# Optimization experiments

Measured on AMD Instinct MI355X. Metric: run time of the kernel, lower is better.

## Reference

```python
import jax, jax.numpy as jnp
import numpy as np


def setup_inputs() -> dict:
    key = jax.random.key(0)
    ks = jax.random.split(key, 6)
    b, t, s, qu, vu, d = 8, 64, 512, 512, 512, 512
    return {
        "query": jax.random.normal(ks[0], (b, t, qu), jnp.float32),
        "value": jax.random.normal(ks[1], (b, s, vu), jnp.float32),
        "mask": jax.random.randint(ks[2], (b, s), 0, 2).astype(bool),
        "W1_w": jax.random.normal(ks[3], (qu, d), jnp.float32) * (1.0 / np.sqrt(qu)),
        "W1_b": jnp.zeros((d,), jnp.float32),
        "W2_w": jax.random.normal(ks[4], (vu, d), jnp.float32) * (1.0 / np.sqrt(vu)),
        "W2_b": jnp.zeros((d,), jnp.float32),
        "scale": jax.random.normal(ks[5], (d,), jnp.float32) * 0.05,
    }


def reference(query, value, mask, W1_w, W1_b, W2_w, W2_b, scale):
    # Dense projections
    q = jnp.einsum('btq,qd->btd', query, W1_w) + W1_b   # [b,t,d]
    k = jnp.einsum('bsv,vd->bsd', value, W2_w) + W2_b   # [b,s,d]
    # Additive (Bahdanau) score with learned scale vector (Keras use_scale=True)
    # scores[b,t,s] = sum_d scale[d] * tanh(q[b,t,d] + k[b,s,d])
    scores = jnp.einsum('btsd,d->bts', jnp.tanh(q[:, :, None, :] + k[:, None, :, :]), scale)
    # Mask over source positions (value mask); query mask is all-ones (no-op)
    scores = jnp.where(mask[:, None, :], scores, jnp.float32(-1e9))
    attention_weights = jax.nn.softmax(scores, axis=-1)   # [b,t,s]
    context_vector = jnp.einsum('bts,bsv->btv', attention_weights, value)  # [b,t,vu]
    return context_vector, attention_weights
```

## Files before the change

kernel.cpp:

```cpp
#include <hip/hip_runtime.h>
#include <hip/hip_bf16.h>

#define B_  8
#define T_  64
#define S_  512
#define D_  512

#define QN (512 * 512)
#define KN (4096 * 512)

#define TLOG2E 2.8853900817779268f
#define LOG2E  1.4426950408889634f

typedef __attribute__((ext_vector_type(8))) short bf16x8;
typedef __attribute__((ext_vector_type(4))) float f32x4;

__device__ __forceinline__ unsigned int pk2(float a, float b) {
    float2 f; f.x = a; f.y = b;
    __hip_bfloat162 h = __float22bfloat162_rn(f);
    return *(unsigned int*)&h;
}

__global__ __launch_bounds__(256) void mfma_gemm(
    const float* __restrict__ query, const float* __restrict__ value,
    const float* __restrict__ W1, const float* __restrict__ W2,
    const float* __restrict__ b1, const float* __restrict__ b2,
    float* __restrict__ qproj, float* __restrict__ kproj)
{
    __shared__ __align__(16) unsigned short Ab[64][40];
    __shared__ __align__(16) unsigned short Bs[64][40];

    const int x = blockIdx.x;
    const float *A, *W;
    float* C;
    int tm, tn;
    bool isq;
    if (x < 512) {
        tm = (x & 7) * 8 + ((x >> 3) & 7);
        tn = x >> 6;
        A = value; W = W2; C = kproj; isq = false;
    } else {
        int r = x - 512;
        tm = r >> 3; tn = r & 7;
        A = query; W = W1; C = qproj; isq = true;
    }

    const int tid  = threadIdx.x;
    const int lane = tid & 63;
    const int wid  = tid >> 6;
    const int wm = (wid & 1) * 32, wn = (wid >> 1) * 32;
    const int fm = lane & 15, fq = lane >> 4;

    f32x4 acc00 = {0.f, 0.f, 0.f, 0.f};
    f32x4 acc01 = acc00, acc10 = acc00, acc11 = acc00;

    const int ar = tid >> 2;
    const int ac = (tid & 3) * 8;
    const float* Ag = A + (size_t)(tm * 64 + ar) * 512 + ac;
    const int c0 = (tid & 15) * 4;
    const int kp = (tid >> 4) * 2;
    const float* Wg = W + (size_t)kp * 512 + tn * 64 + c0;

    float4 av0 = *(const float4*)(Ag);
    float4 av1 = *(const float4*)(Ag + 4);
    float4 wv0 = *(const float4*)(Wg);
    float4 wv1 = *(const float4*)(Wg + 512);

    for (int k0 = 0; k0 < 512; k0 += 32) {
        __syncthreads();
        {
            uint4 pa;
            pa.x = pk2(av0.x, av0.y); pa.y = pk2(av0.z, av0.w);
            pa.z = pk2(av1.x, av1.y); pa.w = pk2(av1.z, av1.w);
            *(uint4*)&Ab[ar][ac] = pa;
            *(unsigned int*)&Bs[c0 + 0][kp] = pk2(wv0.x, wv1.x);
            *(unsigned int*)&Bs[c0 + 1][kp] = pk2(wv0.y, wv1.y);
            *(unsigned int*)&Bs[c0 + 2][kp] = pk2(wv0.z, wv1.z);
            *(unsigned int*)&Bs[c0 + 3][kp] = pk2(wv0.w, wv1.w);
        }
        __syncthreads();
        const int kn = (k0 + 32) & 511;
        av0 = *(const float4*)(Ag + kn);
        av1 = *(const float4*)(Ag + kn + 4);
        wv0 = *(const float4*)(Wg + (size_t)kn * 512);
        wv1 = *(const float4*)(Wg + (size_t)kn * 512 + 512);

        bf16x8 a0  = *(const bf16x8*)&Ab[wm + fm][fq * 8];
        bf16x8 a1  = *(const bf16x8*)&Ab[wm + 16 + fm][fq * 8];
        bf16x8 b0  = *(const bf16x8*)&Bs[wn + fm][fq * 8];
        bf16x8 b1v = *(const bf16x8*)&Bs[wn + 16 + fm][fq * 8];
        acc00 = __builtin_amdgcn_mfma_f32_16x16x32_bf16(a0, b0,  acc00, 0, 0, 0);
        acc01 = __builtin_amdgcn_mfma_f32_16x16x32_bf16(a0, b1v, acc01, 0, 0, 0);
        acc10 = __builtin_amdgcn_mfma_f32_16x16x32_bf16(a1, b0,  acc10, 0, 0, 0);
        acc11 = __builtin_amdgcn_mfma_f32_16x16x32_bf16(a1, b1v, acc11, 0, 0, 0);
    }

    const int n0 = tn * 64 + wn + fm;
    const int n1 = n0 + 16;
    float bias0 = 0.f, bias1 = 0.f;
    if (isq) {
        bias0 = b1[n0] + b2[n0];
        bias1 = b1[n1] + b2[n1];
    }
    const int m0 = tm * 64 + wm + fq * 4;
#pragma unroll
    for (int r = 0; r < 4; ++r) {
        C[(size_t)(m0 + r) * 512 + n0]      = (acc00[r] + bias0) * TLOG2E;
        C[(size_t)(m0 + r) * 512 + n1]      = (acc01[r] + bias1) * TLOG2E;
        C[(size_t)(m0 + 16 + r) * 512 + n0] = (acc10[r] + bias0) * TLOG2E;
        C[(size_t)(m0 + 16 + r) * 512 + n1] = (acc11[r] + bias1) * TLOG2E;
    }
}

__global__ __launch_bounds__(512, 2) void fused_attn(
    const float* __restrict__ qproj, const float* __restrict__ kproj,
    const int*   __restrict__ mask,  const float* __restrict__ scale,
    const float* __restrict__ value,
    float* __restrict__ ctx, float* __restrict__ attn)
{
    const int blk = blockIdx.x;
    const int b  = blk & 7;
    const int tp = blk >> 3;
    const size_t row0 = (size_t)(b * T_ + tp * 2);

    __shared__ __align__(16) float q0A[512];
    __shared__ __align__(16) float dA[512];
    __shared__ __align__(16) float cA[512];
    __shared__ __align__(16) float2 wp2[512];
    __shared__ __align__(16) float4 part[2][4][128];
    __shared__ float2 red2[16];

    const int tid  = threadIdx.x;
    const int lane = tid & 63;
    const int wid  = tid >> 6;

    {
        float q0v = qproj[row0 * D_ + tid];
        float q1v = qproj[(row0 + 1) * D_ + tid];
        q0A[tid] = q0v;
        dA[tid]  = __builtin_amdgcn_exp2f(q1v - q0v);
        cA[tid]  = scale[tid];
    }
    __syncthreads();

    const int s = tid;
    const int m = mask[b * S_ + s];
    const float* kr = kproj + (size_t)(b * S_ + s) * D_;
    float p0 = 0.f, p1 = 0.f;

    float4 kf0 = ((const float4*)kr)[0];
    float4 kf1 = ((const float4*)kr)[1];
    float4 kf2 = ((const float4*)kr)[2];
    float4 kf3 = ((const float4*)kr)[3];

#define SC_STEP(K4, DD) do {                                                  \
        float4 q4 = *(const float4*)&q0A[DD];                                 \
        float4 dl = *(const float4*)&dA[DD];                                  \
        float4 c4 = *(const float4*)&cA[DD];                                  \
        float e, ra, rb;                                                      \
        e  = __builtin_amdgcn_exp2f(q4.x + (K4).x);                           \
        ra = __builtin_amdgcn_rcpf(e + 1.0f);                                 \
        rb = __builtin_amdgcn_rcpf(fmaf(e, dl.x, 1.0f));                      \
        p0 = fmaf(c4.x, ra, p0); p1 = fmaf(c4.x, rb, p1);                     \
        e  = __builtin_amdgcn_exp2f(q4.y + (K4).y);                           \
        ra = __builtin_amdgcn_rcpf(e + 1.0f);                                 \
        rb = __builtin_amdgcn_rcpf(fmaf(e, dl.y, 1.0f));                      \
        p0 = fmaf(c4.y, ra, p0); p1 = fmaf(c4.y, rb, p1);                     \
        e  = __builtin_amdgcn_exp2f(q4.z + (K4).z);                           \
        ra = __builtin_amdgcn_rcpf(e + 1.0f);                                 \
        rb = __builtin_amdgcn_rcpf(fmaf(e, dl.z, 1.0f));                      \
        p0 = fmaf(c4.z, ra, p0); p1 = fmaf(c4.z, rb, p1);                     \
        e  = __builtin_amdgcn_exp2f(q4.w + (K4).w);                           \
        ra = __builtin_amdgcn_rcpf(e + 1.0f);                                 \
        rb = __builtin_amdgcn_rcpf(fmaf(e, dl.w, 1.0f));                      \
        p0 = fmaf(c4.w, ra, p0); p1 = fmaf(c4.w, rb, p1);                     \
    } while (0)

    for (int c = 0; c < 32; ++c) {
        const int nx = ((c + 1) & 31) * 16;
        float4 nf0 = ((const float4*)(kr + nx))[0];
        float4 nf1 = ((const float4*)(kr + nx))[1];
        float4 nf2 = ((const float4*)(kr + nx))[2];
        float4 nf3 = ((const float4*)(kr + nx))[3];
        const int d0 = c * 16;
        SC_STEP(kf0, d0);
        SC_STEP(kf1, d0 + 4);
        SC_STEP(kf2, d0 + 8);
        SC_STEP(kf3, d0 + 12);
        kf0 = nf0; kf1 = nf1; kf2 = nf2; kf3 = nf3;
    }
#undef SC_STEP

    float x0 = m ? (-2.0f * p0) : -1e9f;
    float x1 = m ? (-2.0f * p1) : -1e9f;

    float2 mx; mx.x = x0; mx.y = x1;
#pragma unroll
    for (int off = 32; off >= 1; off >>= 1) {
        mx.x = fmaxf(mx.x, __shfl_xor(mx.x, off));
        mx.y = fmaxf(mx.y, __shfl_xor(mx.y, off));
    }
    if (lane == 0) red2[wid] = mx;
    __syncthreads();
    float2 M = red2[0];
#pragma unroll
    for (int i = 1; i < 8; ++i) {
        M.x = fmaxf(M.x, red2[i].x);
        M.y = fmaxf(M.y, red2[i].y);
    }

    float e0 = __builtin_amdgcn_exp2f((x0 - M.x) * LOG2E);
    float e1 = __builtin_amdgcn_exp2f((x1 - M.y) * LOG2E);
    float2 sm; sm.x = e0; sm.y = e1;
#pragma unroll
    for (int off = 32; off >= 1; off >>= 1) {
        sm.x += __shfl_xor(sm.x, off);
        sm.y += __shfl_xor(sm.y, off);
    }
    if (lane == 0) red2[8 + wid] = sm;
    __syncthreads();
    float2 SS = red2[8];
#pragma unroll
    for (int i = 9; i < 16; ++i) {
        SS.x += red2[i].x;
        SS.y += red2[i].y;
    }
    const float inv0 = __builtin_amdgcn_rcpf(SS.x);
    const float inv1 = __builtin_amdgcn_rcpf(SS.y);
    const float w0 = e0 * inv0, w1 = e1 * inv1;

    float2 wpair; wpair.x = w0; wpair.y = w1;
    wp2[s] = wpair;
    attn[row0 * S_ + s]       = w0;
    attn[(row0 + 1) * S_ + s] = w1;
    __syncthreads();

    const int g  = tid >> 7;
    const int v4 = tid & 127;
    const float* vb = value + ((size_t)(b * S_) + g * 128) * D_ + v4 * 4;
    float4 a0; a0.x = 0.f; a0.y = 0.f; a0.z = 0.f; a0.w = 0.f;
    float4 a1 = a0;
#pragma unroll 4
    for (int i = 0; i < 128; ++i) {
        float4 vv = *(const float4*)(vb + (size_t)i * D_);
        float2 w = wp2[g * 128 + i];
        a0.x = fmaf(w.x, vv.x, a0.x); a0.y = fmaf(w.x, vv.y, a0.y);
        a0.z = fmaf(w.x, vv.z, a0.z); a0.w = fmaf(w.x, vv.w, a0.w);
        a1.x = fmaf(w.y, vv.x, a1.x); a1.y = fmaf(w.y, vv.y, a1.y);
        a1.z = fmaf(w.y, vv.z, a1.z); a1.w = fmaf(w.y, vv.w, a1.w);
    }
    part[0][g][v4] = a0;
    part[1][g][v4] = a1;
    __syncthreads();
    if (tid < 256) {
        const int t = tid >> 7, v = tid & 127;
        float4 p0v = part[t][0][v], p1v = part[t][1][v];
        float4 p2v = part[t][2][v], p3v = part[t][3][v];
        float4 o;
        o.x = (p0v.x + p1v.x) + (p2v.x + p3v.x);
        o.y = (p0v.y + p1v.y) + (p2v.y + p3v.y);
        o.z = (p0v.z + p1v.z) + (p2v.z + p3v.z);
        o.w = (p0v.w + p1v.w) + (p2v.w + p3v.w);
        *(float4*)(ctx + (row0 + t) * D_ + v * 4) = o;
    }
}

extern "C" void kernel_launch(void* const* d_in, const int* in_sizes, int n_in,
                              void* d_out, int out_size, void* d_ws, size_t ws_size,
                              hipStream_t stream) {
    const float* query = (const float*)d_in[0];
    const float* value = (const float*)d_in[1];
    const int*   mask  = (const int*)  d_in[2];
    const float* W1w   = (const float*)d_in[3];
    const float* W1b   = (const float*)d_in[4];
    const float* W2w   = (const float*)d_in[5];
    const float* W2b   = (const float*)d_in[6];
    const float* scale = (const float*)d_in[7];

    float* ctx  = (float*)d_out;
    float* attn = (float*)d_out + (size_t)B_ * T_ * D_;

    float* qproj = (float*)d_ws;
    float* kproj = qproj + (size_t)QN;

    mfma_gemm<<<576, 256, 0, stream>>>(query, value, W1w, W2w, W1b, W2b,
                                       qproj, kproj);
    fused_attn<<<256, 512, 0, stream>>>(qproj, kproj, mask, scale, value,
                                        ctx, attn);
}
```

Baseline: 136.3 us.

## Split attention score D-reduction across 1024 threads and double-buffer GEMM LDS

```diff
diff --git a/kernel.cpp b/kernel.cpp
--- a/kernel.cpp
+++ b/kernel.cpp
@@ -27,8 +27,8 @@
     const float* __restrict__ b1, const float* __restrict__ b2,
     float* __restrict__ qproj, float* __restrict__ kproj)
 {
-    __shared__ __align__(16) unsigned short Ab[64][40];
-    __shared__ __align__(16) unsigned short Bs[64][40];
+    __shared__ __align__(16) unsigned short Ab[2][64][40];
+    __shared__ __align__(16) unsigned short Bs[2][64][40];
 
     const int x = blockIdx.x;
     const float *A, *W;
@@ -61,39 +61,52 @@
     const int kp = (tid >> 4) * 2;
     const float* Wg = W + (size_t)kp * 512 + tn * 64 + c0;
 
-    float4 av0 = *(const float4*)(Ag);
-    float4 av1 = *(const float4*)(Ag + 4);
-    float4 wv0 = *(const float4*)(Wg);
-    float4 wv1 = *(const float4*)(Wg + 512);
-
-    for (int k0 = 0; k0 < 512; k0 += 32) {
-        __syncthreads();
-        {
-            uint4 pa;
-            pa.x = pk2(av0.x, av0.y); pa.y = pk2(av0.z, av0.w);
-            pa.z = pk2(av1.x, av1.y); pa.w = pk2(av1.z, av1.w);
-            *(uint4*)&Ab[ar][ac] = pa;
-            *(unsigned int*)&Bs[c0 + 0][kp] = pk2(wv0.x, wv1.x);
-            *(unsigned int*)&Bs[c0 + 1][kp] = pk2(wv0.y, wv1.y);
-            *(unsigned int*)&Bs[c0 + 2][kp] = pk2(wv0.z, wv1.z);
-            *(unsigned int*)&Bs[c0 + 3][kp] = pk2(wv0.w, wv1.w);
-        }
-        __syncthreads();
-        const int kn = (k0 + 32) & 511;
-        av0 = *(const float4*)(Ag + kn);
-        av1 = *(const float4*)(Ag + kn + 4);
-        wv0 = *(const float4*)(Wg + (size_t)kn * 512);
-        wv1 = *(const float4*)(Wg + (size_t)kn * 512 + 512);
-
-        bf16x8 a0  = *(const bf16x8*)&Ab[wm + fm][fq * 8];
-        bf16x8 a1  = *(const bf16x8*)&Ab[wm + 16 + fm][fq * 8];
-        bf16x8 b0  = *(const bf16x8*)&Bs[wn + fm][fq * 8];
-        bf16x8 b1v = *(const bf16x8*)&Bs[wn + 16 + fm][fq * 8];
+    float4 av0, av1, wv0, wv1;
+
+#define STAGE(BUF) do {                                                       \
+        uint4 pa;                                                             \
+        pa.x = pk2(av0.x, av0.y); pa.y = pk2(av0.z, av0.w);                   \
+        pa.z = pk2(av1.x, av1.y); pa.w = pk2(av1.z, av1.w);                   \
+        *(uint4*)&Ab[BUF][ar][ac] = pa;                                       \
+        *(unsigned int*)&Bs[BUF][c0 + 0][kp] = pk2(wv0.x, wv1.x);             \
+        *(unsigned int*)&Bs[BUF][c0 + 1][kp] = pk2(wv0.y, wv1.y);             \
+        *(unsigned int*)&Bs[BUF][c0 + 2][kp] = pk2(wv0.z, wv1.z);             \
+        *(unsigned int*)&Bs[BUF][c0 + 3][kp] = pk2(wv0.w, wv1.w);             \
+    } while (0)
+
+    av0 = *(const float4*)(Ag);
+    av1 = *(const float4*)(Ag + 4);
+    wv0 = *(const float4*)(Wg);
+    wv1 = *(const float4*)(Wg + 512);
+    STAGE(0);
+    av0 = *(const float4*)(Ag + 32);
+    av1 = *(const float4*)(Ag + 36);
+    wv0 = *(const float4*)(Wg + 32 * 512);
+    wv1 = *(const float4*)(Wg + 33 * 512);
+    __syncthreads();
+
+#pragma unroll
+    for (int i = 0; i < 16; ++i) {
+        const int cur = i & 1, nxt = cur ^ 1;
+        bf16x8 a0  = *(const bf16x8*)&Ab[cur][wm + fm][fq * 8];
+        bf16x8 a1  = *(const bf16x8*)&Ab[cur][wm + 16 + fm][fq * 8];
+        bf16x8 b0  = *(const bf16x8*)&Bs[cur][wn + fm][fq * 8];
+        bf16x8 b1v = *(const bf16x8*)&Bs[cur][wn + 16 + fm][fq * 8];
+        if (i < 15) {
+            STAGE(nxt);
+            const int kn = ((i + 2) & 15) * 32;
+            av0 = *(const float4*)(Ag + kn);
+            av1 = *(const float4*)(Ag + kn + 4);
+            wv0 = *(const float4*)(Wg + (size_t)kn * 512);
+            wv1 = *(const float4*)(Wg + (size_t)kn * 512 + 512);
+        }
         acc00 = __builtin_amdgcn_mfma_f32_16x16x32_bf16(a0, b0,  acc00, 0, 0, 0);
         acc01 = __builtin_amdgcn_mfma_f32_16x16x32_bf16(a0, b1v, acc01, 0, 0, 0);
         acc10 = __builtin_amdgcn_mfma_f32_16x16x32_bf16(a1, b0,  acc10, 0, 0, 0);
         acc11 = __builtin_amdgcn_mfma_f32_16x16x32_bf16(a1, b1v, acc11, 0, 0, 0);
-    }
+        __syncthreads();
+    }
+#undef STAGE
 
     const int n0 = tn * 64 + wn + fm;
     const int n1 = n0 + 16;
@@ -112,7 +125,7 @@
     }
 }
 
-__global__ __launch_bounds__(512, 2) void fused_attn(
+__global__ __launch_bounds__(1024) void fused_attn(
     const float* __restrict__ qproj, const float* __restrict__ kproj,
     const int*   __restrict__ mask,  const float* __restrict__ scale,
     const float* __restrict__ value,
@@ -126,15 +139,16 @@
     __shared__ __align__(16) float q0A[512];
     __shared__ __align__(16) float dA[512];
     __shared__ __align__(16) float cA[512];
+    __shared__ __align__(16) float2 pex[512];
     __shared__ __align__(16) float2 wp2[512];
-    __shared__ __align__(16) float4 part[2][4][128];
+    __shared__ __align__(16) float4 part[2][8][128];
     __shared__ float2 red2[16];
 
     const int tid  = threadIdx.x;
     const int lane = tid & 63;
     const int wid  = tid >> 6;
 
-    {
+    if (tid < 512) {
         float q0v = qproj[row0 * D_ + tid];
         float q1v = qproj[(row0 + 1) * D_ + tid];
         q0A[tid] = q0v;
@@ -143,9 +157,11 @@
     }
     __syncthreads();
 
-    const int s = tid;
+    const int s    = tid & 511;
+    const int half = tid >> 9;
+    const int dlo  = half << 8;
     const int m = mask[b * S_ + s];
-    const float* kr = kproj + (size_t)(b * S_ + s) * D_;
+    const float* kr = kproj + (size_t)(b * S_ + s) * D_ + dlo;
     float p0 = 0.f, p1 = 0.f;
 
     float4 kf0 = ((const float4*)kr)[0];
@@ -176,13 +192,13 @@
         p0 = fmaf(c4.w, ra, p0); p1 = fmaf(c4.w, rb, p1);                     \
     } while (0)
 
-    for (int c = 0; c < 32; ++c) {
-        const int nx = ((c + 1) & 31) * 16;
+    for (int c = 0; c < 16; ++c) {
+        const int nx = ((c + 1) & 15) * 16;
         float4 nf0 = ((const float4*)(kr + nx))[0];
         float4 nf1 = ((const float4*)(kr + nx))[1];
         float4 nf2 = ((const float4*)(kr + nx))[2];
         float4 nf3 = ((const float4*)(kr + nx))[3];
-        const int d0 = c * 16;
+        const int d0 = dlo + c * 16;
         SC_STEP(kf0, d0);
         SC_STEP(kf1, d0 + 4);
         SC_STEP(kf2, d0 + 8);
@@ -191,59 +207,70 @@
     }
 #undef SC_STEP
 
-    float x0 = m ? (-2.0f * p0) : -1e9f;
-    float x1 = m ? (-2.0f * p1) : -1e9f;
-
-    float2 mx; mx.x = x0; mx.y = x1;
-#pragma unroll
-    for (int off = 32; off >= 1; off >>= 1) {
-        mx.x = fmaxf(mx.x, __shfl_xor(mx.x, off));
-        mx.y = fmaxf(mx.y, __shfl_xor(mx.y, off));
-    }
-    if (lane == 0) red2[wid] = mx;
-    __syncthreads();
-    float2 M = red2[0];
-#pragma unroll
-    for (int i = 1; i < 8; ++i) {
-        M.x = fmaxf(M.x, red2[i].x);
-        M.y = fmaxf(M.y, red2[i].y);
-    }
-
-    float e0 = __builtin_amdgcn_exp2f((x0 - M.x) * LOG2E);
-    float e1 = __builtin_amdgcn_exp2f((x1 - M.y) * LOG2E);
-    float2 sm; sm.x = e0; sm.y = e1;
-#pragma unroll
-    for (int off = 32; off >= 1; off >>= 1) {
-        sm.x += __shfl_xor(sm.x, off);
-        sm.y += __shfl_xor(sm.y, off);
-    }
-    if (lane == 0) red2[8 + wid] = sm;
-    __syncthreads();
-    float2 SS = red2[8];
-#pragma unroll
-    for (int i = 9; i < 16; ++i) {
-        SS.x += red2[i].x;
-        SS.y += red2[i].y;
-    }
-    const float inv0 = __builtin_amdgcn_rcpf(SS.x);
-    const float inv1 = __builtin_amdgcn_rcpf(SS.y);
-    const float w0 = e0 * inv0, w1 = e1 * inv1;
-
-    float2 wpair; wpair.x = w0; wpair.y = w1;
-    wp2[s] = wpair;
-    attn[row0 * S_ + s]       = w0;
-    attn[(row0 + 1) * S_ + s] = w1;
+    if (half == 1) { float2 pp; pp.x = p0; pp.y = p1; pex[s] = pp; }
+    __syncthreads();
+
+    float x0 = 0.f, x1 = 0.f;
+    if (tid < 512) {
+        float2 ph = pex[s];
+        p0 += ph.x; p1 += ph.y;
+        x0 = m ? (-2.0f * p0) : -1e9f;
+        x1 = m ? (-2.0f * p1) : -1e9f;
+        float2 mx; mx.x = x0; mx.y = x1;
+#pragma unroll
+        for (int off = 32; off >= 1; off >>= 1) {
+            mx.x = fmaxf(mx.x, __shfl_xor(mx.x, off));
+            mx.y = fmaxf(mx.y, __shfl_xor(mx.y, off));
+        }
+        if (lane == 0) red2[wid] = mx;
+    }
+    __syncthreads();
+
+    float e0 = 0.f, e1 = 0.f;
+    if (tid < 512) {
+        float2 M = red2[0];
+#pragma unroll
+        for (int i = 1; i < 8; ++i) {
+            M.x = fmaxf(M.x, red2[i].x);
+            M.y = fmaxf(M.y, red2[i].y);
+        }
+        e0 = __builtin_amdgcn_exp2f((x0 - M.x) * LOG2E);
+        e1 = __builtin_amdgcn_exp2f((x1 - M.y) * LOG2E);
+        float2 sm; sm.x = e0; sm.y = e1;
+#pragma unroll
+        for (int off = 32; off >= 1; off >>= 1) {
+            sm.x += __shfl_xor(sm.x, off);
+            sm.y += __shfl_xor(sm.y, off);
+        }
+        if (lane == 0) red2[8 + wid] = sm;
+    }
+    __syncthreads();
+
+    if (tid < 512) {
+        float2 SS = red2[8];
+#pragma unroll
+        for (int i = 9; i < 16; ++i) {
+            SS.x += red2[i].x;
+            SS.y += red2[i].y;
+        }
+        const float w0 = e0 * __builtin_amdgcn_rcpf(SS.x);
+        const float w1 = e1 * __builtin_amdgcn_rcpf(SS.y);
+        float2 wpair; wpair.x = w0; wpair.y = w1;
+        wp2[s] = wpair;
+        attn[row0 * S_ + s]       = w0;
+        attn[(row0 + 1) * S_ + s] = w1;
+    }
     __syncthreads();
 
     const int g  = tid >> 7;
     const int v4 = tid & 127;
-    const float* vb = value + ((size_t)(b * S_) + g * 128) * D_ + v4 * 4;
+    const float* vb = value + ((size_t)(b * S_) + g * 64) * D_ + v4 * 4;
     float4 a0; a0.x = 0.f; a0.y = 0.f; a0.z = 0.f; a0.w = 0.f;
     float4 a1 = a0;
 #pragma unroll 4
-    for (int i = 0; i < 128; ++i) {
+    for (int i = 0; i < 64; ++i) {
         float4 vv = *(const float4*)(vb + (size_t)i * D_);
-        float2 w = wp2[g * 128 + i];
+        float2 w = wp2[g * 64 + i];
         a0.x = fmaf(w.x, vv.x, a0.x); a0.y = fmaf(w.x, vv.y, a0.y);
         a0.z = fmaf(w.x, vv.z, a0.z); a0.w = fmaf(w.x, vv.w, a0.w);
         a1.x = fmaf(w.y, vv.x, a1.x); a1.y = fmaf(w.y, vv.y, a1.y);
@@ -254,13 +281,12 @@
     __syncthreads();
     if (tid < 256) {
         const int t = tid >> 7, v = tid & 127;
-        float4 p0v = part[t][0][v], p1v = part[t][1][v];
-        float4 p2v = part[t][2][v], p3v = part[t][3][v];
-        float4 o;
-        o.x = (p0v.x + p1v.x) + (p2v.x + p3v.x);
-        o.y = (p0v.y + p1v.y) + (p2v.y + p3v.y);
-        o.z = (p0v.z + p1v.z) + (p2v.z + p3v.z);
-        o.w = (p0v.w + p1v.w) + (p2v.w + p3v.w);
+        float4 o; o.x = 0.f; o.y = 0.f; o.z = 0.f; o.w = 0.f;
+#pragma unroll
+        for (int gg = 0; gg < 8; ++gg) {
+            float4 p = part[t][gg][v];
+            o.x += p.x; o.y += p.y; o.z += p.z; o.w += p.w;
+        }
         *(float4*)(ctx + (row0 + t) * D_ + v * 4) = o;
     }
 }
@@ -285,6 +311,6 @@
 
     mfma_gemm<<<576, 256, 0, stream>>>(query, value, W1w, W2w, W1b, W2b,
                                        qproj, kproj);
-    fused_attn<<<256, 512, 0, stream>>>(qproj, kproj, mask, scale, value,
-                                        ctx, attn);
+    fused_attn<<<256, 1024, 0, stream>>>(qproj, kproj, mask, scale, value,
+                                         ctx, attn);
 }
```

After: 133.8 us. About the same (-1.9%).
